# Kernel tuning notes

Hardware: AMD Instinct MI355X
Metric: run time of the kernel (lower is better)

Reference implementation:

```python
import jax, jax.numpy as jnp
import numpy as np


def setup_inputs() -> dict:
    key = jax.random.key(0)
    k1, k2, k3 = jax.random.split(key, 3)
    B, N, D = 16, 4096, 64
    q = jax.random.normal(k1, (B, N, D), dtype=jnp.float32)
    k = jax.random.normal(k2, (B, N, D), dtype=jnp.float32)
    v = jax.random.normal(k3, (B, N, D), dtype=jnp.float32)
    return {"q": q, "k": k, "v": v}


def reference(q, k, v):
    # attention = softmax(q @ k^T, axis=2)  (scale=None in the torch module,
    # dropout=0.0 is identity)
    scores = jnp.einsum("bnd,bmd->bnm", q, k)          # [B, N, N]
    attention = jax.nn.softmax(scores, axis=2)          # softmax over keys
    context = jnp.einsum("bnm,bmd->bnd", attention, v)  # [B, N, D]
    return (context, attention)
```

## Files before the change

kernel.cpp:

```cpp
#include <hip/hip_runtime.h>
#include <hip/hip_bf16.h>

typedef _Float16 half8 __attribute__((ext_vector_type(8)));
typedef _Float16 half4 __attribute__((ext_vector_type(4)));
typedef short short8 __attribute__((ext_vector_type(8)));
typedef short short4v __attribute__((ext_vector_type(4)));
typedef float f32x4 __attribute__((ext_vector_type(4)));

#define BATCH 16
#define SEQ   4096
#define DIM   64
#define KVB   64
#define NCH   (SEQ / KVB)
#define NP2   32
#define NP1   8
#define EL_CH 4096
#define EL_SC 8192
#define EL_P1 32768
#define EL_B  (NCH * EL_CH)
#define PHS   264

__device__ __forceinline__ short f2bf(float f) {
    unsigned u = __builtin_bit_cast(unsigned, f);
    u += 0x7FFF + ((u >> 16) & 1);
    return (short)(u >> 16);
}
__device__ __forceinline__ float bf2f(short h) {
    return __builtin_bit_cast(float, (unsigned)((unsigned short)h) << 16);
}

__device__ __forceinline__ void gld16(const void* g, void* l) {
    __builtin_amdgcn_global_load_lds(
        (const __attribute__((address_space(1))) unsigned int*)g,
        (__attribute__((address_space(3))) unsigned int*)l, 16, 0, 0);
}

__global__ __launch_bounds__(256) void preconvert(
    const float* __restrict__ k, const float* __restrict__ v,
    _Float16* __restrict__ kh, _Float16* __restrict__ vh)
{
    int f = blockIdx.x * 256 + threadIdx.x;
    int lane = f & 63;
    int sub  = (f >> 6) & 7;
    int ch   = (f >> 9) & 63;
    int bb   = (f >> 15) & 15;
    int isV  = f >> 19;
    int nf = sub >> 1, kk = sub & 1;
    size_t fo = (size_t)(f & ((1 << 19) - 1)) * 8;

    if (!isV) {
        int key = ch * 64 + nf * 16 + (lane & 15);
        int d0  = kk * 32 + (lane >> 4) * 8;
        const float* src = k + (((size_t)bb * SEQ + key) * DIM + d0);
        half8 h8;
        #pragma unroll
        for (int e = 0; e < 8; ++e) h8[e] = (_Float16)src[e];
        *(half8*)(kh + fo) = h8;
    } else {
        int kr0 = kk * 32 + (lane >> 4) * 8;
        int d   = nf * 16 + (lane & 15);
        const float* src = v + (((size_t)bb * SEQ + ch * 64 + kr0) * DIM + d);
        half8 h8;
        #pragma unroll
        for (int e = 0; e < 8; ++e) h8[e] = (_Float16)src[e * DIM];
        *(half8*)(vh + fo) = h8;
    }
}

__global__ __launch_bounds__(512, 2) void attn_main(
    const float* __restrict__ q, const _Float16* __restrict__ kh,
    const _Float16* __restrict__ vh, float* __restrict__ ctx,
    float* __restrict__ att)
{
    __shared__ __align__(16) _Float16 POOL[66560];

    int id = blockIdx.x;
    int bb = (id & 7) + 8 * (id >> 8);
    int qt = (id >> 3) & 31;

    int tid = threadIdx.x;
    int w = tid >> 6, lane = tid & 63, li = lane & 15, h4 = lane >> 4;

    _Float16* Ph = POOL + 32768 + w * (16 * PHS);

    int qrow = qt * 128 + w * 16 + li;
    const float* qp = q + ((size_t)bb * SEQ + qrow) * DIM;
    half8 aq[2];
    #pragma unroll
    for (int kk = 0; kk < 2; ++kk)
        #pragma unroll
        for (int e = 0; e < 8; ++e)
            aq[kk][e] = (_Float16)qp[kk * 32 + h4 * 8 + e];

    const _Float16* khb = kh + (size_t)bb * EL_B;
    const _Float16* vvb = vh + (size_t)bb * EL_B;

    auto qkt = [&](const _Float16* base, f32x4* s) {
        const half8* k8 = (const half8*)base;
        #pragma unroll
        for (int kk = 0; kk < 2; ++kk)
            #pragma unroll
            for (int nf = 0; nf < 4; ++nf)
                s[nf] = __builtin_amdgcn_mfma_f32_16x16x32_f16(
                    k8[(nf * 2 + kk) * 64 + lane], aq[kk], s[nf], 0, 0, 0);
    };

    float ll = 0.f;

    auto stage_p1 = [&](int buf, int sc) {
        const _Float16* g = khb + (size_t)sc * EL_P1 + tid * 8;
        _Float16* d = POOL + buf * EL_P1;
        #pragma unroll
        for (int o = 0; o < 8; ++o)
            gld16(g + o * 4096, d + o * 4096 + w * 512);
    };

    stage_p1(0, 0);
    for (int sc = 0; sc < NP1; ++sc) {
        int buf = sc & 1;
        if (sc + 1 < NP1) {
            stage_p1(buf ^ 1, sc + 1);
            asm volatile("s_waitcnt vmcnt(8)" ::: "memory");
        } else {
            asm volatile("s_waitcnt vmcnt(0)" ::: "memory");
        }
        __builtin_amdgcn_s_barrier();
        asm volatile("" ::: "memory");

        #pragma unroll
        for (int c8 = 0; c8 < 8; ++c8) {
            f32x4 s[4];
            #pragma unroll
            for (int nf = 0; nf < 4; ++nf) s[nf] = (f32x4){0.f, 0.f, 0.f, 0.f};
            qkt(POOL + buf * EL_P1 + c8 * EL_CH, s);
            float a = 0.f;
            #pragma unroll
            for (int nf = 0; nf < 4; ++nf)
                #pragma unroll
                for (int r = 0; r < 4; ++r)
                    a += __expf(s[nf][r]);
            ll += a;
        }

        asm volatile("" ::: "memory");
        __builtin_amdgcn_s_barrier();
    }

    ll += __shfl_xor(ll, 16);
    ll += __shfl_xor(ll, 32);
    float rl = 1.0f / ll;

    f32x4 acc[4];
    #pragma unroll
    for (int nf = 0; nf < 4; ++nf) acc[nf] = (f32x4){0.f, 0.f, 0.f, 0.f};

    float* attb = att + ((size_t)bb * SEQ + (size_t)qt * 128 + w * 16) * SEQ;

    auto stage_k2 = [&](int buf, int sc) {
        const _Float16* g = khb + (size_t)sc * EL_SC + tid * 8;
        _Float16* d = POOL + buf * EL_SC;
        gld16(g,        d + w * 512);
        gld16(g + 4096, d + 4096 + w * 512);
    };
    auto stage_v2 = [&](int buf, int sc) {
        const _Float16* g = vvb + (size_t)sc * EL_SC + tid * 8;
        _Float16* d = POOL + 16384 + buf * EL_SC;
        gld16(g,        d + w * 512);
        gld16(g + 4096, d + 4096 + w * 512);
    };
    auto store_pair = [&](int p) {
        #pragma unroll
        for (int row = 0; row < 16; ++row) {
            half4 ph = *(const half4*)&Ph[row * PHS + lane * 4];
            f32x4 pv = { (float)ph[0], (float)ph[1], (float)ph[2], (float)ph[3] };
            __builtin_nontemporal_store(
                pv, (f32x4*)(attb + (size_t)row * SEQ + p * 256 + lane * 4));
        }
    };

    stage_k2(0, 0); stage_v2(0, 0);
    for (int sc = 0; sc < NP2; ++sc) {
        int buf = sc & 1;
        if (sc + 1 < NP2) {
            stage_k2(buf ^ 1, sc + 1);
            stage_v2(buf ^ 1, sc + 1);
        }
        if (sc >= 2 && (sc & 1) == 0) store_pair(sc / 2 - 1);

        if (sc < 2)            asm volatile("s_waitcnt vmcnt(4)"  ::: "memory");
        else if (sc + 1 < NP2) asm volatile("s_waitcnt vmcnt(20)" ::: "memory");
        else                   asm volatile("s_waitcnt vmcnt(16)" ::: "memory");
        __builtin_amdgcn_s_barrier();
        asm volatile("" ::: "memory");

        const _Float16* kc = POOL + buf * EL_SC;
        f32x4 sA[4], sB[4];
        #pragma unroll
        for (int nf = 0; nf < 4; ++nf) {
            sA[nf] = (f32x4){0.f, 0.f, 0.f, 0.f};
            sB[nf] = (f32x4){0.f, 0.f, 0.f, 0.f};
        }
        qkt(kc,         sA);
        qkt(kc + EL_CH, sB);

        int slot = (sc & 1) * 128;
        #pragma unroll
        for (int nf = 0; nf < 4; ++nf) {
            half4 pa, pb;
            #pragma unroll
            for (int r = 0; r < 4; ++r) {
                pa[r] = (_Float16)(__expf(sA[nf][r]) * rl);
                pb[r] = (_Float16)(__expf(sB[nf][r]) * rl);
            }
            *(half4*)&Ph[li * PHS + slot + nf * 16 + h4 * 4]      = pa;
            *(half4*)&Ph[li * PHS + slot + 64 + nf * 16 + h4 * 4] = pb;
        }

        const half8* v8 = (const half8*)(POOL + 16384 + buf * EL_SC);
        #pragma unroll
        for (int kk = 0; kk < 4; ++kk) {
            half8 pa = *(const half8*)&Ph[li * PHS + slot + kk * 32 + h4 * 8];
            #pragma unroll
            for (int nf = 0; nf < 4; ++nf)
                acc[nf] = __builtin_amdgcn_mfma_f32_16x16x32_f16(
                    pa, v8[(kk >> 1) * 512 + (nf * 2 + (kk & 1)) * 64 + lane],
                    acc[nf], 0, 0, 0);
        }

        asm volatile("" ::: "memory");
        __builtin_amdgcn_s_barrier();
    }
    store_pair(NP2 / 2 - 1);

    __syncthreads();
    float* Phf = (float*)(POOL + 32768) + w * (16 * 68);
    #pragma unroll
    for (int nf = 0; nf < 4; ++nf)
        #pragma unroll
        for (int r = 0; r < 4; ++r)
            Phf[(4 * h4 + r) * 68 + nf * 16 + li] = acc[nf][r];
    __syncthreads();
    float* ctxw = ctx + ((size_t)bb * SEQ + (size_t)qt * 128 + w * 16) * DIM;
    #pragma unroll
    for (int j = 0; j < 4; ++j) {
        int row = j * 4 + (lane >> 4);
        f32x4 cv = *(const f32x4*)&Phf[row * 68 + (lane & 15) * 4];
        __builtin_nontemporal_store(
            cv, (f32x4*)(ctxw + (size_t)row * DIM + (lane & 15) * 4));
    }
}

__global__ __launch_bounds__(256) void attn_fallback(
    const float* __restrict__ q, const float* __restrict__ k,
    const float* __restrict__ v, float* __restrict__ ctx,
    float* __restrict__ att)
{
    __shared__ short K_hi[KVB][72];
    __shared__ short K_lo[KVB][72];
    __shared__ short V_lds[DIM][72];
    __shared__ short P_lds[4][16][72];

    int id = blockIdx.x;
    int bb = (id & 7) + 8 * (id >> 9);
    int qt = (id >> 3) & 63;
    int tid = threadIdx.x;
    int w = tid >> 6, lane = tid & 63, li = lane & 15, h4 = lane >> 4;

    int qrow = qt * 64 + w * 16 + li;
    const float* qp = q + ((size_t)bb * SEQ + qrow) * DIM;
    short8 aq[2], aql[2];
    #pragma unroll
    for (int kk = 0; kk < 2; ++kk)
        #pragma unroll
        for (int e = 0; e < 8; ++e) {
            float x = qp[kk * 32 + h4 * 8 + e];
            short h = f2bf(x);
            aq[kk][e] = h; aql[kk][e] = f2bf(x - bf2f(h));
        }

    float m[4], l[4];
    #pragma unroll
    for (int r = 0; r < 4; ++r) { m[r] = -3.0e38f; l[r] = 0.0f; }
    const float* kbase = k + (size_t)bb * SEQ * DIM;
    const float* vbase = v + (size_t)bb * SEQ * DIM;

    for (int ch = 0; ch < NCH; ++ch) {
        __syncthreads();
        const float4* kc = (const float4*)(kbase + (size_t)ch * KVB * DIM);
        #pragma unroll
        for (int j = 0; j < 4; ++j) {
            int f4 = j * 256 + tid; int key = f4 >> 4, d4 = f4 & 15;
            float4 val = kc[f4];
            short4v h4v, l4v;
            h4v[0]=f2bf(val.x); l4v[0]=f2bf(val.x-bf2f(h4v[0]));
            h4v[1]=f2bf(val.y); l4v[1]=f2bf(val.y-bf2f(h4v[1]));
            h4v[2]=f2bf(val.z); l4v[2]=f2bf(val.z-bf2f(h4v[2]));
            h4v[3]=f2bf(val.w); l4v[3]=f2bf(val.w-bf2f(h4v[3]));
            *(short4v*)&K_hi[key][d4*4] = h4v;
            *(short4v*)&K_lo[key][d4*4] = l4v;
        }
        __syncthreads();
        f32x4 s[4];
        #pragma unroll
        for (int nf = 0; nf < 4; ++nf) s[nf] = (f32x4){0.f,0.f,0.f,0.f};
        #pragma unroll
        for (int kk = 0; kk < 2; ++kk)
            #pragma unroll
            for (int nf = 0; nf < 4; ++nf) {
                short8 kbv = *(const short8*)&K_hi[nf*16+li][kk*32+h4*8];
                short8 klv = *(const short8*)&K_lo[nf*16+li][kk*32+h4*8];
                s[nf] = __builtin_amdgcn_mfma_f32_16x16x32_bf16(aq[kk],  kbv, s[nf],0,0,0);
                s[nf] = __builtin_amdgcn_mfma_f32_16x16x32_bf16(aq[kk],  klv, s[nf],0,0,0);
                s[nf] = __builtin_amdgcn_mfma_f32_16x16x32_bf16(aql[kk], kbv, s[nf],0,0,0);
            }
        #pragma unroll
        for (int r = 0; r < 4; ++r) {
            float cmax = fmaxf(fmaxf(s[0][r],s[1][r]), fmaxf(s[2][r],s[3][r]));
            #pragma unroll
            for (int off = 1; off < 16; off <<= 1) cmax = fmaxf(cmax, __shfl_xor(cmax, off));
            float mnew = fmaxf(m[r], cmax);
            float cs = __expf(s[0][r]-mnew)+__expf(s[1][r]-mnew)+__expf(s[2][r]-mnew)+__expf(s[3][r]-mnew);
            #pragma unroll
            for (int off = 1; off < 16; off <<= 1) cs += __shfl_xor(cs, off);
            l[r] = l[r]*__expf(m[r]-mnew) + cs; m[r] = mnew;
        }
    }
    float rl[4];
    #pragma unroll
    for (int r = 0; r < 4; ++r) rl[r] = 1.0f / l[r];

    f32x4 acc[4];
    #pragma unroll
    for (int nf = 0; nf < 4; ++nf) acc[nf] = (f32x4){0.f,0.f,0.f,0.f};
    float* attb = att + ((size_t)bb * SEQ + (size_t)qt * 64 + w * 16) * SEQ;

    for (int ch = 0; ch < NCH; ++ch) {
        __syncthreads();
        const float4* kc = (const float4*)(kbase + (size_t)ch * KVB * DIM);
        #pragma unroll
        for (int j = 0; j < 4; ++j) {
            int f4 = j * 256 + tid; int key = f4 >> 4, d4 = f4 & 15;
            float4 val = kc[f4];
            short4v h4v, l4v;
            h4v[0]=f2bf(val.x); l4v[0]=f2bf(val.x-bf2f(h4v[0]));
            h4v[1]=f2bf(val.y); l4v[1]=f2bf(val.y-bf2f(h4v[1]));
            h4v[2]=f2bf(val.z); l4v[2]=f2bf(val.z-bf2f(h4v[2]));
            h4v[3]=f2bf(val.w); l4v[3]=f2bf(val.w-bf2f(h4v[3]));
            *(short4v*)&K_hi[key][d4*4] = h4v;
            *(short4v*)&K_lo[key][d4*4] = l4v;
        }
        {
            int key = tid & 63, dblk = (tid >> 6) * 16;
            const float* vc = vbase + ((size_t)ch * KVB + key) * DIM + dblk;
            #pragma unroll
            for (int j = 0; j < 4; ++j) {
                float4 val = *(const float4*)(vc + j * 4);
                V_lds[dblk+j*4+0][key]=f2bf(val.x); V_lds[dblk+j*4+1][key]=f2bf(val.y);
                V_lds[dblk+j*4+2][key]=f2bf(val.z); V_lds[dblk+j*4+3][key]=f2bf(val.w);
            }
        }
        __syncthreads();
        f32x4 s[4];
        #pragma unroll
        for (int nf = 0; nf < 4; ++nf) s[nf] = (f32x4){0.f,0.f,0.f,0.f};
        #pragma unroll
        for (int kk = 0; kk < 2; ++kk)
            #pragma unroll
            for (int nf = 0; nf < 4; ++nf) {
                short8 kbv = *(const short8*)&K_hi[nf*16+li][kk*32+h4*8];
                short8 klv = *(const short8*)&K_lo[nf*16+li][kk*32+h4*8];
                s[nf] = __builtin_amdgcn_mfma_f32_16x16x32_bf16(aq[kk],  kbv, s[nf],0,0,0);
                s[nf] = __builtin_amdgcn_mfma_f32_16x16x32_bf16(aq[kk],  klv, s[nf],0,0,0);
                s[nf] = __builtin_amdgcn_mfma_f32_16x16x32_bf16(aql[kk], kbv, s[nf],0,0,0);
            }
        #pragma unroll
        for (int nf = 0; nf < 4; ++nf)
            #pragma unroll
            for (int r = 0; r < 4; ++r) {
                float p = __expf(s[nf][r] - m[r]) * rl[r];
                __builtin_nontemporal_store(p, &attb[(size_t)(4*h4+r)*SEQ + ch*KVB + nf*16 + li]);
                P_lds[w][4*h4+r][nf*16+li] = f2bf(p);
            }
        #pragma unroll
        for (int kk = 0; kk < 2; ++kk) {
            short8 pa = *(const short8*)&P_lds[w][li][kk*32+h4*8];
            #pragma unroll
            for (int nf = 0; nf < 4; ++nf) {
                short8 vbv = *(const short8*)&V_lds[nf*16+li][kk*32+h4*8];
                acc[nf] = __builtin_amdgcn_mfma_f32_16x16x32_bf16(pa, vbv, acc[nf],0,0,0);
            }
        }
    }
    float* ctxb = ctx + ((size_t)bb * SEQ + (size_t)qt * 64 + w * 16) * DIM;
    #pragma unroll
    for (int nf = 0; nf < 4; ++nf)
        #pragma unroll
        for (int r = 0; r < 4; ++r)
            __builtin_nontemporal_store(acc[nf][r], &ctxb[(size_t)(4*h4+r)*DIM + nf*16 + li]);
}

extern "C" void kernel_launch(void* const* d_in, const int* in_sizes, int n_in,
                              void* d_out, int out_size, void* d_ws, size_t ws_size,
                              hipStream_t stream) {
    const float* q = (const float*)d_in[0];
    const float* k = (const float*)d_in[1];
    const float* v = (const float*)d_in[2];
    float* ctx = (float*)d_out;
    float* att = (float*)d_out + (size_t)BATCH * SEQ * DIM;

    const size_t t_el = (size_t)BATCH * EL_B;
    const size_t need = 2 * t_el * 2;

    if (ws_size >= need) {
        _Float16* kh = (_Float16*)d_ws;
        _Float16* vh = kh + t_el;
        preconvert<<<4096, 256, 0, stream>>>(k, v, kh, vh);
        attn_main<<<512, 512, 0, stream>>>(q, kh, vh, ctx, att);
    } else {
        attn_fallback<<<BATCH * (SEQ / 64), 256, 0, stream>>>(q, k, v, ctx, att);
    }
}
```

Measured before the change: 260.1 us.

## Process two query tiles per block to reuse staged K/V and halve grid

Each block now handles 256 query rows as two 128-row halves that share every staged K and V chunk, so K/V traffic from global memory into LDS per query row is halved and the grid drops to 256 blocks. The attention-probability store is reworked to write each 128-column tile right after computing it, replacing the deferred paired store, and the P staging stride shrinks. The cost is more registers (two accumulators and two Q fragments), fewer blocks than the 256 CUs can usefully overlap (one block per CU), and loss of the previous overlap between attention stores and the next tile's loads.

```diff
diff --git a/kernel.cpp b/kernel.cpp
--- a/kernel.cpp
+++ b/kernel.cpp
@@ -18,7 +18,7 @@
 #define EL_SC 8192
 #define EL_P1 32768
 #define EL_B  (NCH * EL_CH)
-#define PHS   264
+#define PHS   136
 
 __device__ __forceinline__ short f2bf(float f) {
     unsigned u = __builtin_bit_cast(unsigned, f);
@@ -72,30 +72,33 @@
     const _Float16* __restrict__ vh, float* __restrict__ ctx,
     float* __restrict__ att)
 {
-    __shared__ __align__(16) _Float16 POOL[66560];
+    __shared__ __align__(16) _Float16 POOL[65536];
 
     int id = blockIdx.x;
-    int bb = (id & 7) + 8 * (id >> 8);
-    int qt = (id >> 3) & 31;
+    int bb = (id & 7) + 8 * (id >> 7);
+    int qt = (id >> 3) & 15;
 
     int tid = threadIdx.x;
     int w = tid >> 6, lane = tid & 63, li = lane & 15, h4 = lane >> 4;
 
     _Float16* Ph = POOL + 32768 + w * (16 * PHS);
 
-    int qrow = qt * 128 + w * 16 + li;
-    const float* qp = q + ((size_t)bb * SEQ + qrow) * DIM;
-    half8 aq[2];
+    int rowA = qt * 256 + w * 16 + li;
+    const float* qpA = q + ((size_t)bb * SEQ + rowA) * DIM;
+    const float* qpB = qpA + (size_t)128 * DIM;
+    half8 aqA[2], aqB[2];
     #pragma unroll
     for (int kk = 0; kk < 2; ++kk)
         #pragma unroll
-        for (int e = 0; e < 8; ++e)
-            aq[kk][e] = (_Float16)qp[kk * 32 + h4 * 8 + e];
+        for (int e = 0; e < 8; ++e) {
+            aqA[kk][e] = (_Float16)qpA[kk * 32 + h4 * 8 + e];
+            aqB[kk][e] = (_Float16)qpB[kk * 32 + h4 * 8 + e];
+        }
 
     const _Float16* khb = kh + (size_t)bb * EL_B;
     const _Float16* vvb = vh + (size_t)bb * EL_B;
 
-    auto qkt = [&](const _Float16* base, f32x4* s) {
+    auto qkt = [&](const _Float16* base, const half8* aq, f32x4* s) {
         const half8* k8 = (const half8*)base;
         #pragma unroll
         for (int kk = 0; kk < 2; ++kk)
@@ -105,7 +108,7 @@
                     k8[(nf * 2 + kk) * 64 + lane], aq[kk], s[nf], 0, 0, 0);
     };
 
-    float ll = 0.f;
+    float llA = 0.f, llB = 0.f;
 
     auto stage_p1 = [&](int buf, int sc) {
         const _Float16* g = khb + (size_t)sc * EL_P1 + tid * 8;
@@ -129,32 +132,46 @@
 
         #pragma unroll
         for (int c8 = 0; c8 < 8; ++c8) {
+            const _Float16* base = POOL + buf * EL_P1 + c8 * EL_CH;
             f32x4 s[4];
             #pragma unroll
             for (int nf = 0; nf < 4; ++nf) s[nf] = (f32x4){0.f, 0.f, 0.f, 0.f};
-            qkt(POOL + buf * EL_P1 + c8 * EL_CH, s);
+            qkt(base, aqA, s);
             float a = 0.f;
             #pragma unroll
             for (int nf = 0; nf < 4; ++nf)
                 #pragma unroll
-                for (int r = 0; r < 4; ++r)
-                    a += __expf(s[nf][r]);
-            ll += a;
+                for (int r = 0; r < 4; ++r) a += __expf(s[nf][r]);
+            llA += a;
+
+            #pragma unroll
+            for (int nf = 0; nf < 4; ++nf) s[nf] = (f32x4){0.f, 0.f, 0.f, 0.f};
+            qkt(base, aqB, s);
+            float b = 0.f;
+            #pragma unroll
+            for (int nf = 0; nf < 4; ++nf)
+                #pragma unroll
+                for (int r = 0; r < 4; ++r) b += __expf(s[nf][r]);
+            llB += b;
         }
 
         asm volatile("" ::: "memory");
         __builtin_amdgcn_s_barrier();
     }
 
-    ll += __shfl_xor(ll, 16);
-    ll += __shfl_xor(ll, 32);
-    float rl = 1.0f / ll;
-
-    f32x4 acc[4];
-    #pragma unroll
-    for (int nf = 0; nf < 4; ++nf) acc[nf] = (f32x4){0.f, 0.f, 0.f, 0.f};
-
-    float* attb = att + ((size_t)bb * SEQ + (size_t)qt * 128 + w * 16) * SEQ;
+    llA += __shfl_xor(llA, 16); llA += __shfl_xor(llA, 32);
+    llB += __shfl_xor(llB, 16); llB += __shfl_xor(llB, 32);
+    float rlA = 1.0f / llA, rlB = 1.0f / llB;
+
+    f32x4 accA[4], accB[4];
+    #pragma unroll
+    for (int nf = 0; nf < 4; ++nf) {
+        accA[nf] = (f32x4){0.f, 0.f, 0.f, 0.f};
+        accB[nf] = (f32x4){0.f, 0.f, 0.f, 0.f};
+    }
+
+    float* attbA = att + ((size_t)bb * SEQ + (size_t)qt * 256 + w * 16) * SEQ;
+    float* attbB = attbA + (size_t)128 * SEQ;
 
     auto stage_k2 = [&](int buf, int sc) {
         const _Float16* g = khb + (size_t)sc * EL_SC + tid * 8;
@@ -168,13 +185,48 @@
         gld16(g,        d + w * 512);
         gld16(g + 4096, d + 4096 + w * 512);
     };
-    auto store_pair = [&](int p) {
-        #pragma unroll
-        for (int row = 0; row < 16; ++row) {
-            half4 ph = *(const half4*)&Ph[row * PHS + lane * 4];
+
+    auto do_tile = [&](const _Float16* kc, const half8* v8, const half8* aq,
+                       float rl, float* attb, int sc, f32x4* acc) {
+        f32x4 sA[4], sB[4];
+        #pragma unroll
+        for (int nf = 0; nf < 4; ++nf) {
+            sA[nf] = (f32x4){0.f, 0.f, 0.f, 0.f};
+            sB[nf] = (f32x4){0.f, 0.f, 0.f, 0.f};
+        }
+        qkt(kc,         aq, sA);
+        qkt(kc + EL_CH, aq, sB);
+
+        #pragma unroll
+        for (int nf = 0; nf < 4; ++nf) {
+            half4 pa, pb;
+            #pragma unroll
+            for (int r = 0; r < 4; ++r) {
+                pa[r] = (_Float16)(__expf(sA[nf][r]) * rl);
+                pb[r] = (_Float16)(__expf(sB[nf][r]) * rl);
+            }
+            *(half4*)&Ph[li * PHS + nf * 16 + h4 * 4]      = pa;
+            *(half4*)&Ph[li * PHS + 64 + nf * 16 + h4 * 4] = pb;
+        }
+
+        #pragma unroll
+        for (int j = 0; j < 8; ++j) {
+            int row = j * 2 + (lane >> 5);
+            int col = (lane & 31) * 4;
+            half4 ph = *(const half4*)&Ph[row * PHS + col];
             f32x4 pv = { (float)ph[0], (float)ph[1], (float)ph[2], (float)ph[3] };
             __builtin_nontemporal_store(
-                pv, (f32x4*)(attb + (size_t)row * SEQ + p * 256 + lane * 4));
+                pv, (f32x4*)(attb + (size_t)row * SEQ + sc * 128 + col));
+        }
+
+        #pragma unroll
+        for (int kk = 0; kk < 4; ++kk) {
+            half8 pa = *(const half8*)&Ph[li * PHS + kk * 32 + h4 * 8];
+            #pragma unroll
+            for (int nf = 0; nf < 4; ++nf)
+                acc[nf] = __builtin_amdgcn_mfma_f32_16x16x32_f16(
+                    pa, v8[(kk >> 1) * 512 + (nf * 2 + (kk & 1)) * 64 + lane],
+                    acc[nf], 0, 0, 0);
         }
     };
 
@@ -184,69 +236,44 @@
         if (sc + 1 < NP2) {
             stage_k2(buf ^ 1, sc + 1);
             stage_v2(buf ^ 1, sc + 1);
-        }
-        if (sc >= 2 && (sc & 1) == 0) store_pair(sc / 2 - 1);
-
-        if (sc < 2)            asm volatile("s_waitcnt vmcnt(4)"  ::: "memory");
-        else if (sc + 1 < NP2) asm volatile("s_waitcnt vmcnt(20)" ::: "memory");
-        else                   asm volatile("s_waitcnt vmcnt(16)" ::: "memory");
+            if (sc == 0) asm volatile("s_waitcnt vmcnt(4)"  ::: "memory");
+            else         asm volatile("s_waitcnt vmcnt(20)" ::: "memory");
+        } else {
+            asm volatile("s_waitcnt vmcnt(16)" ::: "memory");
+        }
         __builtin_amdgcn_s_barrier();
         asm volatile("" ::: "memory");
 
         const _Float16* kc = POOL + buf * EL_SC;
-        f32x4 sA[4], sB[4];
-        #pragma unroll
-        for (int nf = 0; nf < 4; ++nf) {
-            sA[nf] = (f32x4){0.f, 0.f, 0.f, 0.f};
-            sB[nf] = (f32x4){0.f, 0.f, 0.f, 0.f};
-        }
-        qkt(kc,         sA);
-        qkt(kc + EL_CH, sB);
-
-        int slot = (sc & 1) * 128;
-        #pragma unroll
-        for (int nf = 0; nf < 4; ++nf) {
-            half4 pa, pb;
-            #pragma unroll
-            for (int r = 0; r < 4; ++r) {
-                pa[r] = (_Float16)(__expf(sA[nf][r]) * rl);
-                pb[r] = (_Float16)(__expf(sB[nf][r]) * rl);
-            }
-            *(half4*)&Ph[li * PHS + slot + nf * 16 + h4 * 4]      = pa;
-            *(half4*)&Ph[li * PHS + slot + 64 + nf * 16 + h4 * 4] = pb;
-        }
-
         const half8* v8 = (const half8*)(POOL + 16384 + buf * EL_SC);
-        #pragma unroll
-        for (int kk = 0; kk < 4; ++kk) {
-            half8 pa = *(const half8*)&Ph[li * PHS + slot + kk * 32 + h4 * 8];
-            #pragma unroll
-            for (int nf = 0; nf < 4; ++nf)
-                acc[nf] = __builtin_amdgcn_mfma_f32_16x16x32_f16(
-                    pa, v8[(kk >> 1) * 512 + (nf * 2 + (kk & 1)) * 64 + lane],
-                    acc[nf], 0, 0, 0);
-        }
+        do_tile(kc, v8, aqA, rlA, attbA, sc, accA);
+        do_tile(kc, v8, aqB, rlB, attbB, sc, accB);
 
         asm volatile("" ::: "memory");
         __builtin_amdgcn_s_barrier();
     }
-    store_pair(NP2 / 2 - 1);
 
     __syncthreads();
     float* Phf = (float*)(POOL + 32768) + w * (16 * 68);
-    #pragma unroll
-    for (int nf = 0; nf < 4; ++nf)
-        #pragma unroll
-        for (int r = 0; r < 4; ++r)
-            Phf[(4 * h4 + r) * 68 + nf * 16 + li] = acc[nf][r];
-    __syncthreads();
-    float* ctxw = ctx + ((size_t)bb * SEQ + (size_t)qt * 128 + w * 16) * DIM;
-    #pragma unroll
-    for (int j = 0; j < 4; ++j) {
-        int row = j * 4 + (lane >> 4);
-        f32x4 cv = *(const f32x4*)&Phf[row * 68 + (lane & 15) * 4];
-        __builtin_nontemporal_store(
-            cv, (f32x4*)(ctxw + (size_t)row * DIM + (lane & 15) * 4));
+    float* ctxwA = ctx + ((size_t)bb * SEQ + (size_t)qt * 256 + w * 16) * DIM;
+    #pragma unroll
+    for (int t = 0; t < 2; ++t) {
+        f32x4* acc = t ? accB : accA;
+        float* ctxw = ctxwA + (size_t)t * 128 * DIM;
+        #pragma unroll
+        for (int nf = 0; nf < 4; ++nf)
+            #pragma unroll
+            for (int r = 0; r < 4; ++r)
+                Phf[(4 * h4 + r) * 68 + nf * 16 + li] = acc[nf][r];
+        asm volatile("s_waitcnt lgkmcnt(0)" ::: "memory");
+        #pragma unroll
+        for (int j = 0; j < 4; ++j) {
+            int row = j * 4 + (lane >> 4);
+            f32x4 cv = *(const f32x4*)&Phf[row * 68 + (lane & 15) * 4];
+            __builtin_nontemporal_store(
+                cv, (f32x4*)(ctxw + (size_t)row * DIM + (lane & 15) * 4));
+        }
+        asm volatile("s_waitcnt lgkmcnt(0)" ::: "memory");
     }
 }
 
@@ -415,7 +442,7 @@
         _Float16* kh = (_Float16*)d_ws;
         _Float16* vh = kh + t_el;
         preconvert<<<4096, 256, 0, stream>>>(k, v, kh, vh);
-        attn_main<<<512, 512, 0, stream>>>(q, kh, vh, ctx, att);
+        attn_main<<<256, 512, 0, stream>>>(q, kh, vh, ctx, att);
     } else {
         attn_fallback<<<BATCH * (SEQ / 64), 256, 0, stream>>>(q, k, v, ctx, att);
     }
```

Measured after the change: 249.0 us. 1.04x faster.
